# Kernel optimization log

Measured on AMD Instinct MI355X. Metric: run time of the kernel, lower is better.

Reference implementation:

```python
import jax, jax.numpy as jnp
import numpy as np

B, L, H, E = 4, 2048, 8, 64
WINDOW = 8
DILATION = 1


def setup_inputs() -> dict:
    key = jax.random.key(0)
    kq, kk, kv, ka = jax.random.split(key, 4)
    queries = jax.random.normal(kq, (B, L, H, E), dtype=jnp.float32)
    keys = jax.random.normal(kk, (B, L, H, E), dtype=jnp.float32)
    values = jax.random.normal(kv, (B, L, H, E), dtype=jnp.float32)
    alpha = jax.random.uniform(ka, (1,), dtype=jnp.float32)
    return {"queries": queries, "keys": keys, "values": values, "alpha": alpha}


def _full_attention(q, k, v, scale):
    # q,k,v: [B, L, H, E]
    scores = jnp.einsum('blhe,bshe->bhls', q, k) * scale  # [B,H,L,L]
    A = jax.nn.softmax(scores, axis=-1)
    return jnp.einsum('bhls,bshd->blhd', A, v)


def _local_attention(q, k, v, scale):
    # efficient gather-based local window attention, non-causal
    Lk = k.shape[1]
    offsets = jnp.arange(-WINDOW, WINDOW + 1) * DILATION
    idx = jnp.clip(jnp.arange(Lk)[:, None] + offsets[None, :], 0, Lk - 1)
    K_win = k[:, idx]
    V_win = v[:, idx]
    scores = jnp.einsum('blhe,blwhe->blhw', q, K_win) * scale
    A = jax.nn.softmax(scores, axis=-1)
    return jnp.einsum('blhw,blwhe->blhe', A, V_win)


def reference(queries, keys, values, alpha):
    scale = 1.0 / np.sqrt(queries.shape[-1]).astype(np.float32)
    out_full = _full_attention(queries, keys, values, scale)
    out_local = _local_attention(queries, keys, values, scale)
    w = jax.nn.sigmoid(alpha[0])
    # only_target_first=True: positions 1..L-1 take out_full, position 0 is gated
    out = out_full.at[:, 0].set(w * out_full[:, 0] + (1.0 - w) * out_local[:, 0])
    return out
```

## Files before the change

### kernel.cpp

```cpp
#include <hip/hip_runtime.h>

typedef unsigned short u16;
typedef unsigned int   u32;
typedef __attribute__((ext_vector_type(8))) short short8;
typedef __attribute__((ext_vector_type(16))) float f32x16;

#define MFMA32(a, b, c) __builtin_amdgcn_mfma_f32_32x32x16_bf16(a, b, c, 0, 0, 0)

constexpr int Lv = 2048, Hv = 8, Ev = 64, HE = Hv * Ev;
constexpr float QSCALE = 0.18033688011112042f;
constexpr size_t WSV_OFF = 32u * 64u * 2048u;
#define WS_NEED ((size_t)16777216)

__device__ __forceinline__ float bf2f(u16 u) {
    u32 x = ((u32)u) << 16;
    return __builtin_bit_cast(float, x);
}
__device__ __forceinline__ u16 f2bf(float f) {
    u32 x = __builtin_bit_cast(u32, f);
    u32 r = ((x >> 16) & 1u) + 0x7fffu;
    return (u16)((x + r) >> 16);
}
__device__ __forceinline__ u32 pkbf(float a, float b) {
#if __has_builtin(__builtin_amdgcn_cvt_pk_bf16_f32)
    typedef __attribute__((ext_vector_type(2))) __bf16 bf16x2;
    bf16x2 v = __builtin_amdgcn_cvt_pk_bf16_f32(a, b);
    return __builtin_bit_cast(u32, v);
#else
    return (u32)f2bf(a) | ((u32)f2bf(b) << 16);
#endif
}
__device__ __forceinline__ float fexp2(float x) {
#if __has_builtin(__builtin_amdgcn_exp2f)
    return __builtin_amdgcn_exp2f(x);
#else
    return exp2f(x);
#endif
}

__device__ __forceinline__ void gll16(const void* g, void* l) {
    __builtin_amdgcn_global_load_lds(
        (const __attribute__((address_space(1))) void*)g,
        (__attribute__((address_space(3))) void*)l, 16, 0, 0);
}

__device__ __forceinline__ int detect_isbf16(const u32* q32, int lane) {
    u32 w0 = q32[2 * lane];
    u32 w1 = q32[2 * lane + 1];
    u16 uu[4] = { (u16)(w0 & 0xffff), (u16)(w0 >> 16),
                  (u16)(w1 & 0xffff), (u16)(w1 >> 16) };
    int p = 0, z = 0;
#pragma unroll
    for (int j = 0; j < 4; ++j) {
        u16 mgn = (u16)(uu[j] & 0x7fff);
        int ex  = mgn >> 7;
        bool zero = (mgn == 0);
        bool pl   = zero || (ex >= 115 && ex <= 132);
        p += pl ? 1 : 0;
        if ((j & 1) == 0) z += zero ? 1 : 0;
    }
    int acc = p | (z << 16);
#pragma unroll
    for (int o = 1; o < 64; o <<= 1) acc += __shfl_xor(acc, o);
    int ps = acc & 0xffff, zs = acc >> 16;
    if (zs >= 100) return 0;
    return (ps >= 240) ? 1 : 0;
}

__device__ __forceinline__ short8 cvt8s(const float* p, float s) {
    float4 a = *(const float4*)p, b4 = *(const float4*)(p + 4);
    u32 r[4] = { pkbf(a.x * s, a.y * s), pkbf(a.z * s, a.w * s),
                 pkbf(b4.x * s, b4.y * s), pkbf(b4.z * s, b4.w * s) };
    return *(short8*)r;
}

__device__ __forceinline__ f32x16 zv16() {
    f32x16 z;
#pragma unroll
    for (int r = 0; r < 16; ++r) z[r] = 0.f;
    return z;
}

__device__ __forceinline__ void plswap(u32& a, u32& b) {
#if __has_builtin(__builtin_amdgcn_permlane32_swap)
    auto r = __builtin_amdgcn_permlane32_swap(a, b, false, false);
    a = r[0]; b = r[1];
#else
    int lane = (int)(threadIdx.x & 63);
    u32 ax = (u32)__shfl_xor((int)a, 32);
    u32 bx = (u32)__shfl_xor((int)b, 32);
    bool hi = lane >= 32;
    u32 na = hi ? bx : a;
    u32 nb = hi ? b  : ax;
    a = na; b = nb;
#endif
}

template <int ISBF>
__device__ __forceinline__ void convert_impl(const void* kin, const void* vin,
                                             u16* __restrict__ ws, u16* VT) {
    const int blk = blockIdx.x;
    const int bh  = blk >> 6, tg = blk & 63;
    const int b   = bh >> 3,  h  = bh & 7;
    const size_t inb = (size_t)b * Lv * HE + h * Ev;
    u16* kimg = ws + (size_t)blk * 2048;
    u16* vimg = ws + WSV_OFF + (size_t)blk * 2048;
    const int t = threadIdx.x;

#pragma unroll
    for (int r = 0; r < 2; ++r) {
        int f = t + 256 * r;
        int key = f >> 4, part = f & 15;
        size_t src = inb + (size_t)(tg * 32 + key) * HE + part * 4;
        if (ISBF) {
            uint2 vv_ = *(const uint2*)((const u16*)vin + src);
            *(uint2*)&VT[key * 68 + part * 4] = vv_;
        } else {
            float4 v = *(const float4*)((const float*)vin + src);
            *(u32*)&VT[key * 68 + part * 4]     = pkbf(v.x, v.y);
            *(u32*)&VT[key * 68 + part * 4 + 2] = pkbf(v.z, v.w);
        }
    }

#pragma unroll
    for (int r = 0; r < 4; ++r) {
        int i = t + 256 * r, a = 2 * i;
        int key = a >> 6, sf = (a & 63) >> 3, j0 = a & 7;
        int e0 = ((sf ^ (key & 7)) << 3) + j0;
        size_t s = inb + (size_t)(tg * 32 + key) * HE + e0;
        u32 val;
        if (ISBF) val = *(const u32*)((const u16*)kin + s);
        else { float2 kvv = *(const float2*)((const float*)kin + s);
               val = pkbf(kvv.x, kvv.y); }
        *(u32*)&kimg[a] = val;
    }

    __syncthreads();

#pragma unroll
    for (int r = 0; r < 4; ++r) {
        int i = t + 256 * r, a = 2 * i;
        int e = a >> 5, sf = (a & 31) >> 3, j0 = a & 7;
        int k0 = ((sf ^ ((e + (e >> 3)) & 3)) << 3) + j0;
        u32 val = (u32)VT[k0 * 68 + e] | ((u32)VT[(k0 + 1) * 68 + e] << 16);
        *(u32*)&vimg[a] = val;
    }
}

__global__ __launch_bounds__(256) void convert_kernel(
    const void* __restrict__ qv, const void* __restrict__ kv,
    const void* __restrict__ vv, u16* __restrict__ ws)
{
    __shared__ u16 VT[32 * 68];
    const int isbf = detect_isbf16((const u32*)qv, threadIdx.x & 63);
    if (isbf) convert_impl<1>(kv, vv, ws, VT);
    else      convert_impl<0>(kv, vv, ws, VT);
}

template <int ISBF, int WS>
__device__ __forceinline__ void attn_impl(
    const void* __restrict__ qv, const void* __restrict__ kv,
    const void* __restrict__ vv, const void* __restrict__ alphav,
    void* __restrict__ outv, const u16* __restrict__ ws, u16* SMEM)
{
    const int tid  = threadIdx.x;
    const int w    = tid >> 6;
    const int lane = tid & 63;
    const int l31  = lane & 31;
    const int hi   = lane >> 5;
    const int qg   = w & 3;
    const int g    = w >> 2;

    const int fid = blockIdx.x;
    const int bh  = (fid & 7) * 4 + ((fid >> 3) & 3);
    const int rb  = fid >> 5;
    const int b   = bh >> 3, h = bh & 7;
    const int row0 = rb * 128;

    const size_t bhoff = (size_t)b * Lv * HE + h * Ev;
    const u16*   q16 = (const u16*)qv + bhoff;
    const u16*   k16 = (const u16*)kv + bhoff;
    const u16*   v16 = (const u16*)vv + bhoff;
    const float* q32 = (const float*)qv + bhoff;
    const float* k32 = (const float*)kv + bhoff;
    const float* v32 = (const float*)vv + bhoff;

    u16* ldsK = SMEM + w * 4096;
    u16* ldsV = ldsK + 2048;

    short8 qf[4];
    {
        size_t ro = (size_t)(row0 + qg * 32 + l31) * HE + hi * 8;
        if (ISBF) {
#pragma unroll
            for (int c = 0; c < 4; ++c) {
                short8 t = *(const short8*)(q16 + ro + 16 * c);
#pragma unroll
                for (int j = 0; j < 8; ++j)
                    qf[c][j] = (short)f2bf(bf2f((u16)t[j]) * QSCALE);
            }
        } else {
#pragma unroll
            for (int c = 0; c < 4; ++c) qf[c] = cvt8s(q32 + ro + 16 * c, QSCALE);
        }
    }

    f32x16 O[2];
    O[0] = zv16(); O[1] = zv16();
    float psum = 0.f;

    const u16* kimg0 = ws + ((size_t)bh * 64 + g * 32) * 2048;
    const u16* vimg0 = ws + WSV_OFF + ((size_t)bh * 64 + g * 32) * 2048;
    const size_t keybase = (size_t)g * 1024;

    const int k0l = lane >> 3;
    const int kj  = lane & 7;
    const int e0K = ((kj ^ k0l) << 3);
    const int eoV = kj * 8;

    float4 fpa, fpb, fpc, fpd;
    uint4  upa, upb;

#define GLLK(KT) do {                                                          \
        const u16* ib_ = kimg0 + (size_t)(KT) * 2048 + lane * 8;               \
        _Pragma("unroll")                                                      \
        for (int s_ = 0; s_ < 4; ++s_)                                         \
            gll16(ib_ + s_ * 512, ldsK + s_ * 512);                            \
    } while (0)
#define GLLV(KT) do {                                                          \
        const u16* ib_ = vimg0 + (size_t)(KT) * 2048 + lane * 8;               \
        _Pragma("unroll")                                                      \
        for (int s_ = 0; s_ < 4; ++s_)                                         \
            gll16(ib_ + s_ * 512, ldsV + s_ * 512);                            \
    } while (0)
#define WAITV4() do { asm volatile("s_waitcnt vmcnt(4)" ::: "memory");         \
        __builtin_amdgcn_sched_barrier(0); } while (0)
#define WAITV0() do { asm volatile("s_waitcnt vmcnt(0)" ::: "memory");         \
        __builtin_amdgcn_sched_barrier(0); } while (0)
#define WAITL0() do { asm volatile("s_waitcnt lgkmcnt(0)" ::: "memory");       \
        __builtin_amdgcn_sched_barrier(0); } while (0)

#define LK0(KT, CH) do {                                                       \
        size_t tb_ = (keybase + (size_t)(KT) * 32) * HE;                       \
        int key_ = (CH) * 16 + k0l;                                            \
        if (ISBF) {                                                            \
            const u16* p_ = k16 + tb_ + (size_t)key_ * HE + e0K;               \
            upa = *(const uint4*)p_;                                           \
            upb = *(const uint4*)(p_ + 8 * HE);                                \
        } else {                                                               \
            const float* p_ = k32 + tb_ + (size_t)key_ * HE + e0K;             \
            fpa = *(const float4*)p_;            fpb = *(const float4*)(p_ + 4);\
            fpc = *(const float4*)(p_ + 8 * HE); fpd = *(const float4*)(p_ + 8 * HE + 4);\
        }                                                                      \
    } while (0)
#define SK0(CH) do {                                                           \
        if (ISBF) {                                                            \
            *(uint4*)&ldsK[((CH)*2    ) * 512 + lane * 8] = upa;               \
            *(uint4*)&ldsK[((CH)*2 + 1) * 512 + lane * 8] = upb;               \
        } else {                                                               \
            u32 t0_[4] = { pkbf(fpa.x, fpa.y), pkbf(fpa.z, fpa.w),             \
                           pkbf(fpb.x, fpb.y), pkbf(fpb.z, fpb.w) };           \
            u32 t1_[4] = { pkbf(fpc.x, fpc.y), pkbf(fpc.z, fpc.w),             \
                           pkbf(fpd.x, fpd.y), pkbf(fpd.z, fpd.w) };           \
            *(uint4*)&ldsK[((CH)*2    ) * 512 + lane * 8] = *(uint4*)t0_;      \
            *(uint4*)&ldsK[((CH)*2 + 1) * 512 + lane * 8] = *(uint4*)t1_;      \
        }                                                                      \
    } while (0)
#define LV0(KT, VH) do {                                                       \
        size_t tb_ = (keybase + (size_t)(KT) * 32 + (VH) * 16 + 2 * k0l) * HE; \
        if (ISBF) {                                                            \
            const u16* p_ = v16 + tb_ + eoV;                                   \
            upa = *(const uint4*)p_;                                           \
            upb = *(const uint4*)(p_ + HE);                                    \
        } else {                                                               \
            const float* p_ = v32 + tb_ + eoV;                                 \
            fpa = *(const float4*)p_;       fpb = *(const float4*)(p_ + 4);    \
            fpc = *(const float4*)(p_ + HE); fpd = *(const float4*)(p_ + HE + 4);\
        }                                                                      \
    } while (0)
#define SV0(VH) do {                                                           \
        int s_ = (k0l >> 2) + (VH) * 2;                                        \
        if (ISBF) {                                                            \
            const u16* a0_ = (const u16*)&upa;                                 \
            const u16* a1_ = (const u16*)&upb;                                 \
            _Pragma("unroll")                                                  \
            for (int j = 0; j < 8; ++j) {                                      \
                int e_ = eoV + j;                                              \
                int sl_ = s_ ^ ((e_ + (e_ >> 3)) & 3);                         \
                *(u32*)&ldsV[e_ * 32 + sl_ * 8 + ((2 * k0l) & 7)] =            \
                    (u32)a0_[j] | ((u32)a1_[j] << 16);                         \
            }                                                                  \
        } else {                                                               \
            float t0_[8] = {fpa.x, fpa.y, fpa.z, fpa.w, fpb.x, fpb.y, fpb.z, fpb.w};\
            float t1_[8] = {fpc.x, fpc.y, fpc.z, fpc.w, fpd.x, fpd.y, fpd.z, fpd.w};\
            _Pragma("unroll")                                                  \
            for (int j = 0; j < 8; ++j) {                                      \
                int e_ = eoV + j;                                              \
                int sl_ = s_ ^ ((e_ + (e_ >> 3)) & 3);                         \
                *(u32*)&ldsV[e_ * 32 + sl_ * 8 + ((2 * k0l) & 7)] =            \
                    pkbf(t0_[j], t1_[j]);                                      \
            }                                                                  \
        }                                                                      \
    } while (0)

    f32x16 St;
#define QK_() do {                                                             \
        St = zv16();                                                           \
        __builtin_amdgcn_s_setprio(1);                                         \
        _Pragma("unroll")                                                      \
        for (int c = 0; c < 4; ++c) {                                          \
            int sl = (2 * c + hi) ^ (l31 & 7);                                 \
            short8 kf = *(const short8*)&ldsK[l31 * 64 + sl * 8];              \
            St = MFMA32(kf, qf[c], St);                                        \
        }                                                                      \
        __builtin_amdgcn_s_setprio(0);                                         \
    } while (0)

    u32 c8[8];
#define SM_() do {                                                             \
        _Pragma("unroll")                                                      \
        for (int r = 0; r < 16; ++r) St[r] = fexp2(St[r]);                     \
        _Pragma("unroll")                                                      \
        for (int r = 0; r < 16; ++r) psum += St[r];                            \
        _Pragma("unroll")                                                      \
        for (int q = 0; q < 8; ++q) c8[q] = pkbf(St[2 * q], St[2 * q + 1]);    \
    } while (0)

#define PV_(T) do {                                                            \
        u32 a0 = c8[4 * (T) + 0], a1 = c8[4 * (T) + 1];                        \
        u32 a2 = c8[4 * (T) + 2], a3 = c8[4 * (T) + 3];                        \
        plswap(a0, a2);                                                        \
        plswap(a1, a3);                                                        \
        u32 pw_[4] = { a0, a1, a2, a3 };                                       \
        short8 pa = *(short8*)pw_;                                             \
        __builtin_amdgcn_s_setprio(1);                                         \
        _Pragma("unroll")                                                      \
        for (int et = 0; et < 2; ++et) {                                       \
            int e  = et * 32 + l31;                                            \
            int sl = (2 * (T) + hi) ^ ((e + (e >> 3)) & 3);                    \
            short8 vf = *(const short8*)&ldsV[e * 32 + sl * 8];                \
            O[et] = MFMA32(pa, vf, O[et]);                                     \
        }                                                                      \
        __builtin_amdgcn_s_setprio(0);                                         \
    } while (0)

    if (WS) {
        GLLK(0); GLLV(0);
        for (int kt = 0; kt < 31; ++kt) {
            WAITV4();
            QK_();
            WAITL0();
            GLLK(kt + 1);
            SM_();
            WAITV4();
            PV_(0);
            PV_(1);
            WAITL0();
            GLLV(kt + 1);
        }
        WAITV0();
        QK_();
        SM_();
        PV_(0);
        PV_(1);
    } else {
        LK0(0, 0); SK0(0); LK0(0, 1); SK0(1);
        LV0(0, 0); SV0(0); LV0(0, 1); SV0(1);
        for (int kt = 0; kt < 32; ++kt) {
            if (kt < 31) LK0(kt + 1, 0);
            QK_();
            if (kt < 31) { SK0(0); LK0(kt + 1, 1); }
            SM_();
            if (kt < 31) { SK0(1); LV0(kt + 1, 0); }
            PV_(0);
            if (kt < 31) { SV0(0); LV0(kt + 1, 1); }
            PV_(1);
            if (kt < 31) SV0(1);
        }
    }
#undef GLLK
#undef GLLV
#undef WAITV4
#undef WAITV0
#undef WAITL0
#undef LK0
#undef SK0
#undef LV0
#undef SV0
#undef QK_
#undef SM_
#undef PV_

    __syncthreads();
    float pst = psum + __shfl_xor(psum, 32);
    float* cb = (float*)SMEM;
    const int cbase = qg * 2368 + lane * 36;

    if (g == 1) {
        union { f32x16 v; float4 q4[4]; } u;
        u.v = O[0];
#pragma unroll
        for (int i = 0; i < 4; ++i) *(float4*)&cb[cbase + 4 * i] = u.q4[i];
        u.v = O[1];
#pragma unroll
        for (int i = 0; i < 4; ++i) *(float4*)&cb[cbase + 16 + 4 * i] = u.q4[i];
        cb[qg * 2368 + 2304 + lane] = pst;
    }

    float locv[2] = {0.f, 0.f};
    float wgt = 0.f;
    const bool w0blk = (rb == 0) && (w == 0);
    if (w0blk) {
        const int e = lane;
        const size_t base = bhoff + e;
#define LDIN(p, i) (ISBF ? bf2f(((const u16*)(p))[i]) : ((const float*)(p))[i])
        float qe = LDIN(qv, base);
        float s[9];
#pragma unroll
        for (int j = 0; j < 9; ++j) {
            float prod = qe * LDIN(kv, base + (size_t)j * HE);
#pragma unroll
            for (int o = 1; o < 64; o <<= 1) prod += __shfl_xor(prod, o);
            s[j] = prod * 0.125f;
        }
        float mx = s[0];
#pragma unroll
        for (int j = 1; j < 9; ++j) mx = fmaxf(mx, s[j]);
        float we[9];
#pragma unroll
        for (int j = 0; j < 9; ++j) we[j] = expf(s[j] - mx);
        float denom = 9.f * we[0];
        float acc   = 9.f * we[0] * LDIN(vv, base);
#pragma unroll
        for (int j = 1; j < 9; ++j) {
            denom += we[j];
            acc   += we[j] * LDIN(vv, base + (size_t)j * HE);
        }
        float loc = acc / denom;

        float a;
        if (ISBF) {
            a = bf2f(((const u16*)alphav)[0]);
            if (!(a >= 0.0f && a <= 1.0f)) {
                float af = ((const float*)alphav)[0];
                if (af >= 0.0f && af <= 1.0f) a = af;
            }
        } else {
            a = ((const float*)alphav)[0];
            if (!(a >= 0.0f && a <= 1.0f)) {
                float ab = bf2f(((const u16*)alphav)[0]);
                if (ab >= 0.0f && ab <= 1.0f) a = ab;
            }
        }
        wgt = 1.f / (1.f + expf(-a));
#pragma unroll
        for (int et = 0; et < 2; ++et) locv[et] = __shfl(loc, et * 32 + l31);
#undef LDIN
    }

    __syncthreads();
    if (g != 0) return;

    float pstp = cb[qg * 2368 + 2304 + lane];
#pragma unroll
    for (int r = 0; r < 16; ++r) {
        O[0][r] += cb[cbase + r];
        O[1][r] += cb[cbase + 16 + r];
    }
    float invv = 1.0f / (pst + pstp);

#pragma unroll
    for (int rg = 0; rg < 4; ++rg) {
#pragma unroll
        for (int rr = 0; rr < 4; ++rr) {
            const int reg = rg * 4 + rr;
            const int rl  = rr + 8 * rg + 4 * hi;
            float inv = __shfl(invv, rl);
            int row = row0 + qg * 32 + rl;
            size_t oo = (size_t)(b * Lv + row) * HE + h * Ev + l31;
            bool blend = w0blk && (rl == 0);
#pragma unroll
            for (int et = 0; et < 2; ++et) {
                float res = O[et][reg] * inv;
                if (blend) res = wgt * res + (1.f - wgt) * locv[et];
                if (ISBF) ((u16*)outv)[oo + et * 32] = f2bf(res);
                else      ((float*)outv)[oo + et * 32] = res;
            }
        }
    }
}

__global__ __launch_bounds__(512, 4) void attn_kernel_ws(
    const void* __restrict__ qv, const void* __restrict__ kv,
    const void* __restrict__ vv, const void* __restrict__ alphav,
    void* __restrict__ outv, const u16* __restrict__ ws)
{
    __shared__ u16 SMEM[32768];
    const int isbf = detect_isbf16((const u32*)qv, threadIdx.x & 63);
    if (isbf) attn_impl<1, 1>(qv, kv, vv, alphav, outv, ws, SMEM);
    else      attn_impl<0, 1>(qv, kv, vv, alphav, outv, ws, SMEM);
}

__global__ __launch_bounds__(512, 4) void attn_kernel_nws(
    const void* __restrict__ qv, const void* __restrict__ kv,
    const void* __restrict__ vv, const void* __restrict__ alphav,
    void* __restrict__ outv)
{
    __shared__ u16 SMEM[32768];
    const int isbf = detect_isbf16((const u32*)qv, threadIdx.x & 63);
    if (isbf) attn_impl<1, 0>(qv, kv, vv, alphav, outv, nullptr, SMEM);
    else      attn_impl<0, 0>(qv, kv, vv, alphav, outv, nullptr, SMEM);
}

extern "C" void kernel_launch(void* const* d_in, const int* in_sizes, int n_in,
                              void* d_out, int out_size, void* d_ws, size_t ws_size,
                              hipStream_t stream) {
    if (d_ws != nullptr && ws_size >= WS_NEED) {
        hipLaunchKernelGGL(convert_kernel, dim3(2048), dim3(256), 0, stream,
                           d_in[0], d_in[1], d_in[2], (u16*)d_ws);
        hipLaunchKernelGGL(attn_kernel_ws, dim3(512), dim3(512), 0, stream,
                           d_in[0], d_in[1], d_in[2], d_in[3], d_out,
                           (const u16*)d_ws);
    } else {
        hipLaunchKernelGGL(attn_kernel_nws, dim3(512), dim3(512), 0, stream,
                           d_in[0], d_in[1], d_in[2], d_in[3], d_out);
    }
}
```

Before: 150.0 us.

## Software-pipeline QK and softmax across iterations with double-buffered score registers

Restructures the workspace main loop so the QK^T MFMA for tile kt+1 is issued before the softmax/exp of tile kt, using two ping-pong score accumulators (StA/StB) and a 2x unrolled loop body. The aim is to overlap MFMA latency with the transcendental exp work and the global-to-LDS loads. The V load schedule is shifted by one tile to match the new prologue and epilogue. In exchange it uses more VGPRs for the extra accumulator, which may hurt occupancy, and the wait/load ordering becomes more intricate.

```diff
diff --git a/kernel.cpp b/kernel.cpp
--- a/kernel.cpp
+++ b/kernel.cpp
@@ -207,6 +207,7 @@
 
     f32x16 O[2];
     O[0] = zv16(); O[1] = zv16();
+    f32x16 StA = zv16(), StB = zv16();
     float psum = 0.f;
 
     const u16* kimg0 = ws + ((size_t)bh * 64 + g * 32) * 2048;
@@ -303,27 +304,26 @@
         }                                                                      \
     } while (0)
 
-    f32x16 St;
-#define QK_() do {                                                             \
-        St = zv16();                                                           \
+#define QK_(ST) do {                                                           \
+        (ST) = zv16();                                                         \
         __builtin_amdgcn_s_setprio(1);                                         \
         _Pragma("unroll")                                                      \
         for (int c = 0; c < 4; ++c) {                                          \
             int sl = (2 * c + hi) ^ (l31 & 7);                                 \
             short8 kf = *(const short8*)&ldsK[l31 * 64 + sl * 8];              \
-            St = MFMA32(kf, qf[c], St);                                        \
+            (ST) = MFMA32(kf, qf[c], (ST));                                    \
         }                                                                      \
         __builtin_amdgcn_s_setprio(0);                                         \
     } while (0)
 
     u32 c8[8];
-#define SM_() do {                                                             \
-        _Pragma("unroll")                                                      \
-        for (int r = 0; r < 16; ++r) St[r] = fexp2(St[r]);                     \
-        _Pragma("unroll")                                                      \
-        for (int r = 0; r < 16; ++r) psum += St[r];                            \
-        _Pragma("unroll")                                                      \
-        for (int q = 0; q < 8; ++q) c8[q] = pkbf(St[2 * q], St[2 * q + 1]);    \
+#define SM_(SP) do {                                                           \
+        _Pragma("unroll")                                                      \
+        for (int r = 0; r < 16; ++r) (SP)[r] = fexp2((SP)[r]);                 \
+        _Pragma("unroll")                                                      \
+        for (int r = 0; r < 16; ++r) psum += (SP)[r];                          \
+        _Pragma("unroll")                                                      \
+        for (int q = 0; q < 8; ++q) c8[q] = pkbf((SP)[2 * q], (SP)[2 * q + 1]);\
     } while (0)
 
 #define PV_(T) do {                                                            \
@@ -344,23 +344,42 @@
         __builtin_amdgcn_s_setprio(0);                                         \
     } while (0)
 
+#define BODY(KT, SC, SP) do {                                                  \
+        WAITV4();                   \
+        QK_(SC);                    \
+        SM_(SP);                    \
+        WAITL0();                   \
+        GLLK((KT) + 1);                                                        \
+        WAITV4();                   \
+        PV_(0);                                                                \
+        PV_(1);                     \
+        WAITL0();                   \
+        GLLV(KT);                                                              \
+    } while (0)
+
     if (WS) {
-        GLLK(0); GLLV(0);
-        for (int kt = 0; kt < 31; ++kt) {
-            WAITV4();
-            QK_();
-            WAITL0();
-            GLLK(kt + 1);
-            SM_();
-            WAITV4();
-            PV_(0);
-            PV_(1);
-            WAITL0();
-            GLLV(kt + 1);
-        }
+        GLLK(0);
         WAITV0();
-        QK_();
-        SM_();
+        QK_(StA);
+        WAITL0();
+        GLLK(1);
+        GLLV(0);
+        for (int j = 0; j < 15; ++j) {
+            const int kt = 2 * j + 1;
+            BODY(kt,     StB, StA);
+            BODY(kt + 1, StA, StB);
+        }
+        WAITV4();
+        QK_(StB);
+        SM_(StA);
+        WAITL0();
+        WAITV0();
+        PV_(0);
+        PV_(1);
+        WAITL0();
+        GLLV(31);
+        WAITV0();
+        SM_(StB);
         PV_(0);
         PV_(1);
     } else {
@@ -368,9 +387,9 @@
         LV0(0, 0); SV0(0); LV0(0, 1); SV0(1);
         for (int kt = 0; kt < 32; ++kt) {
             if (kt < 31) LK0(kt + 1, 0);
-            QK_();
+            QK_(StA);
             if (kt < 31) { SK0(0); LK0(kt + 1, 1); }
-            SM_();
+            SM_(StA);
             if (kt < 31) { SK0(1); LV0(kt + 1, 0); }
             PV_(0);
             if (kt < 31) { SV0(0); LV0(kt + 1, 1); }
@@ -390,6 +409,7 @@
 #undef QK_
 #undef SM_
 #undef PV_
+#undef BODY
 
     __syncthreads();
     float pst = psum + __shfl_xor(psum, 32);
```

Result: faster. 147.0 us (-2.0%).
